# Performance work log

Measured on AMD Instinct MI355X. Metric: run time of the kernel, lower is better.

## Reference

```python
import jax, jax.numpy as jnp
import numpy as np

D_MODEL = 1024
NUM_HEADS = 16
D_K = D_MODEL // NUM_HEADS
TEMPERATURE = 1.0
EPS = 1e-6


def setup_inputs() -> dict:
    key = jax.random.key(0)
    ks = jax.random.split(key, 8)
    B, S, D, H = 2, 2048, D_MODEL, NUM_HEADS
    sc = 1.0 / np.sqrt(D)
    x = jax.random.normal(ks[0], (B, S, D), dtype=jnp.float32)
    Wq = jax.random.normal(ks[1], (D, D), dtype=jnp.float32) * sc
    Wk = jax.random.normal(ks[2], (D, D), dtype=jnp.float32) * sc
    Wv = jax.random.normal(ks[3], (D, D), dtype=jnp.float32) * sc
    Wo = jax.random.normal(ks[4], (D, D), dtype=jnp.float32) * sc
    bo = jnp.zeros((D,), dtype=jnp.float32)
    phase_scale = jnp.ones((H,), dtype=jnp.float32)
    # orthogonal init for entanglement matrix
    q, _ = np.linalg.qr(np.random.default_rng(0).normal(size=(H, H)))
    ent = jnp.asarray(q, dtype=jnp.float32)
    gamma = jnp.ones((D,), dtype=jnp.float32)
    beta = jnp.zeros((D,), dtype=jnp.float32)
    return {"x": x, "Wq": Wq, "Wk": Wk, "Wv": Wv, "Wo": Wo, "bo": bo,
            "phase_scale": phase_scale, "ent": ent, "gamma": gamma, "beta": beta}


def reference(x, Wq, Wk, Wv, Wo, bo, phase_scale, ent, gamma, beta):
    B, S, D = x.shape
    H, dk = NUM_HEADS, D_K
    # projections -> [B, H, S, dk]
    Q = (x @ Wq).reshape(B, S, H, dk).transpose(0, 2, 1, 3)
    K = (x @ Wk).reshape(B, S, H, dk).transpose(0, 2, 1, 3)
    V = (x @ Wv).reshape(B, S, H, dk).transpose(0, 2, 1, 3)
    # per-head QK^T, scaled, phase-modulated
    scores = jnp.einsum('bhqd,bhkd->bhqk', Q, K)
    inv = 1.0 / (float(np.sqrt(dk)) * TEMPERATURE)
    s = scores * (inv * phase_scale)[None, :, None, None]
    # real part of quantum phase: cos(s) + 0.1*cos(2s)  (imag part of V is zero,
    # so head_output = attended_real; the 0.1*attended_imag term vanishes)
    w = jnp.cos(s) + 0.1 * jnp.cos(2.0 * s)
    w = jax.nn.softmax(w, axis=-1)
    att = jnp.einsum('bhqk,bhkd->bhqd', w, V).transpose(0, 2, 1, 3)  # [B,S,H,dk]
    # faithful reproduction of tf.einsum('bsnd,hm->bsmd', ...): sums over n AND h
    att = jnp.einsum('bsnd,hm->bsmd', att, ent)
    out = att.reshape(B, S, D) @ Wo + bo
    r = out + x
    mu = jnp.mean(r, axis=-1, keepdims=True)
    var = jnp.mean(jnp.square(r - mu), axis=-1, keepdims=True)
    return gamma * (r - mu) * jax.lax.rsqrt(var + EPS) + beta
```

## Files before the change

kernel.cpp:

```cpp
#include <hip/hip_runtime.h>
#include <cstdint>
#include <cstddef>

#define S_LEN 2048
#define DMODEL 1024
#define NHEADS 16
#define DKH 64
#define MROWS 4096
#define BH_CNT 32

typedef __bf16 bf16x8 __attribute__((ext_vector_type(8)));
typedef __bf16 bf16x2 __attribute__((ext_vector_type(2)));
typedef float f32x4 __attribute__((ext_vector_type(4)));
typedef unsigned int u32x4 __attribute__((ext_vector_type(4)));
typedef unsigned int u32;
typedef unsigned short u16;

__device__ __forceinline__ u16 f2bfu(float f) {
  u32 u = __float_as_uint(f);
  return (u16)((u + 0x7FFFu + ((u >> 16) & 1u)) >> 16);
}

__device__ __forceinline__ u32 pk_bf16(float a, float b) {
  bf16x2 v;
  v[0] = (__bf16)a;
  v[1] = (__bf16)b;
  return __builtin_bit_cast(u32, v);
}

__device__ __forceinline__ void pl32swap(u32& a, u32& b) {
#if __has_builtin(__builtin_amdgcn_permlane32_swap)
  auto r = __builtin_amdgcn_permlane32_swap((int)a, (int)b, false, false);
  a = (u32)r[0]; b = (u32)r[1];
#else
  asm volatile("v_permlane32_swap_b32 %0, %1" : "+v"(a), "+v"(b));
#endif
}
__device__ __forceinline__ void pl16swap(u32& a, u32& b) {
#if __has_builtin(__builtin_amdgcn_permlane16_swap)
  auto r = __builtin_amdgcn_permlane16_swap((int)a, (int)b, false, false);
  a = (u32)r[0]; b = (u32)r[1];
#else
  asm volatile("v_permlane16_swap_b32 %0, %1" : "+v"(a), "+v"(b));
#endif
}

__device__ __forceinline__ void gload16(void* lds, const void* g) {
  __builtin_amdgcn_global_load_lds(
      (const __attribute__((address_space(1))) void*)g,
      (__attribute__((address_space(3))) void*)lds, 16, 0, 0);
}

__global__ __launch_bounds__(256) void prep_xb_k(const float* __restrict__ x,
                                                 u16* __restrict__ xb) {
  int i = (blockIdx.x * 256 + threadIdx.x) * 4;
  float4 v = *(const float4*)(x + i);
  *(uint2*)(xb + i) = make_uint2(pk_bf16(v.x, v.y), pk_bf16(v.z, v.w));
}

__global__ __launch_bounds__(256) void prep_w_k(const float* __restrict__ Wq,
    const float* __restrict__ Wk, const float* __restrict__ Wv,
    const float* __restrict__ ps, u16* __restrict__ Wb) {
  __shared__ float tile[32][33];
  int sel = blockIdx.z;
  const float* W = sel == 0 ? Wq : (sel == 1 ? Wk : Wv);
  int k0 = blockIdx.x * 32, c0 = blockIdx.y * 32;
  int tx = threadIdx.x, ty = threadIdx.y;
#pragma unroll
  for (int i = 0; i < 4; ++i)
    tile[ty + i * 8][tx] = W[(size_t)(k0 + ty + i * 8) * DMODEL + c0 + tx];
  __syncthreads();
#pragma unroll
  for (int i = 0; i < 4; ++i) {
    int row = ty + i * 8;
    float v = tile[tx][row];
    if (sel == 1) v *= 0.019894367886486918f * ps[(c0 + row) >> 6];
    Wb[(size_t)(sel * 1024 + c0 + row) * DMODEL + k0 + tx] = f2bfu(v);
  }
}

__global__ __launch_bounds__(256) void prep_woeff_k(const float* __restrict__ Wo,
    const float* __restrict__ ent, float* __restrict__ Woeff) {
  __shared__ float e[16];
  int t = threadIdx.x;
  if (t < 16) {
    float s = 0.f;
#pragma unroll
    for (int h = 0; h < 16; ++h) s += ent[h * 16 + t];
    e[t] = s;
  }
  __syncthreads();
  int gid = blockIdx.x * 256 + t;
  int d = gid >> 10, j = gid & 1023;
  float acc = 0.f;
#pragma unroll
  for (int m = 0; m < 16; ++m) acc += e[m] * Wo[(size_t)((m << 6) + d) * DMODEL + j];
  Woeff[(size_t)d * DMODEL + j] = acc;
}

__global__ __launch_bounds__(256) void gemm_qkv_k(const u16* __restrict__ xb,
    const u16* __restrict__ Wb, u16* __restrict__ Qb, u16* __restrict__ Kb,
    u16* __restrict__ Vt) {
  __shared__ __align__(16) u16 SMEM[2][2][128 * 32];
  int bid = blockIdx.x;
  int xcd = bid & 7, wi = bid >> 3;
  int mg = xcd >> 1, ng = xcd & 1;
  int mt = mg * 8 + (wi & 7);
  int nt = ng * 12 + (wi >> 3);
  int m0 = mt * 128, n0 = nt * 128;
  int tid = threadIdx.x;
  int lane = tid & 63, w = tid >> 6;
  int c = lane & 15, g = lane >> 4;
  int wr = w >> 1, wc = w & 1;

  int cij0 = (w * 2) * 64 + lane, cij1 = (w * 2 + 1) * 64 + lane;
  int row0 = cij0 >> 2, kp0 = (cij0 & 3) ^ (row0 & 3);
  int row1 = cij1 >> 2, kp1 = (cij1 & 3) ^ (row1 & 3);
  const u16* a0p = xb + (size_t)(m0 + row0) * DMODEL + kp0 * 8;
  const u16* a1p = xb + (size_t)(m0 + row1) * DMODEL + kp1 * 8;
  const u16* b0p = Wb + (size_t)(n0 + row0) * DMODEL + kp0 * 8;
  const u16* b1p = Wb + (size_t)(n0 + row1) * DMODEL + kp1 * 8;

  f32x4 acc[4][4];
#pragma unroll
  for (int i = 0; i < 4; ++i)
#pragma unroll
    for (int j = 0; j < 4; ++j) acc[i][j] = (f32x4){0.f, 0.f, 0.f, 0.f};

  gload16(&SMEM[0][0][(w * 2) * 512], a0p);
  gload16(&SMEM[0][0][(w * 2 + 1) * 512], a1p);
  gload16(&SMEM[1][0][(w * 2) * 512], b0p);
  gload16(&SMEM[1][0][(w * 2 + 1) * 512], b1p);
  __syncthreads();

  int cur = 0;
  for (int kt = 0; kt < DMODEL; kt += 32) {
    if (kt + 32 < DMODEL) {
      int nx = cur ^ 1, ko = kt + 32;
      gload16(&SMEM[0][nx][(w * 2) * 512], a0p + ko);
      gload16(&SMEM[0][nx][(w * 2 + 1) * 512], a1p + ko);
      gload16(&SMEM[1][nx][(w * 2) * 512], b0p + ko);
      gload16(&SMEM[1][nx][(w * 2 + 1) * 512], b1p + ko);
    }
    const u16* Ac = SMEM[0][cur];
    const u16* Bc = SMEM[1][cur];
    bf16x8 af[4], bf[4];
#pragma unroll
    for (int i = 0; i < 4; ++i) {
      int ra = wr * 64 + i * 16 + c;
      af[i] = *(const bf16x8*)(Ac + ra * 32 + ((g ^ (ra & 3)) * 8));
      int rb = wc * 64 + i * 16 + c;
      bf[i] = *(const bf16x8*)(Bc + rb * 32 + ((g ^ (rb & 3)) * 8));
    }
#pragma unroll
    for (int i = 0; i < 4; ++i)
#pragma unroll
      for (int j = 0; j < 4; ++j)
        acc[i][j] = __builtin_amdgcn_mfma_f32_16x16x32_bf16(af[i], bf[j], acc[i][j], 0, 0, 0);
    __syncthreads();
    cur ^= 1;
  }

  int sel = n0 >> 10;
  char* Ls = (char*)&SMEM[0][0][0];
  if (sel == 2) {
#pragma unroll
    for (int i = 0; i < 4; ++i)
#pragma unroll
      for (int jf = 0; jf < 4; ++jf) {
        int n = wc * 64 + jf * 16 + c;
        int m = wr * 64 + i * 16 + 4 * g;
        int byte = n * 256 + ((m * 2) ^ ((n & 7) << 4));
        *(uint2*)(Ls + byte) = make_uint2(pk_bf16(acc[i][jf][0], acc[i][jf][1]),
                                          pk_bf16(acc[i][jf][2], acc[i][jf][3]));
      }
  } else {
#pragma unroll
    for (int i = 0; i < 4; ++i)
#pragma unroll
      for (int jf = 0; jf < 4; ++jf) {
        int n = wc * 64 + jf * 16 + c;
#pragma unroll
        for (int j = 0; j < 4; ++j) {
          int m = wr * 64 + i * 16 + 4 * g + j;
          int byte = m * 256 + ((n * 2) ^ ((m & 7) << 4));
          __bf16 hv = (__bf16)acc[i][jf][j];
          *(u16*)(Ls + byte) = __builtin_bit_cast(u16, hv);
        }
      }
  }
  __syncthreads();
  int r = tid >> 1, half = tid & 1;
  int h0 = (n0 & 1023) >> 6;
  int b = m0 >> 11, sbase = m0 & 2047;
  u16* dst;
  if (sel == 2) {
    int bh = b * 16 + h0 + (r >> 6), d = r & 63;
    dst = Vt + ((size_t)bh * DKH + d) * S_LEN + sbase + half * 64;
  } else {
    u16* base = (sel == 0 ? Qb : Kb);
    int bh = b * 16 + h0 + half;
    dst = base + ((size_t)bh * S_LEN + sbase + r) * DKH;
  }
#pragma unroll
  for (int kk = 0; kk < 8; ++kk) {
    int byte = r * 256 + ((half * 128 + kk * 16) ^ ((r & 7) << 4));
    *(uint4*)(dst + kk * 8) = *(const uint4*)(Ls + byte);
  }
}

__global__ __launch_bounds__(512) void attn_k(const u16* __restrict__ Qb,
    const u16* __restrict__ Kb, const u16* __restrict__ Vt,
    float* __restrict__ attbuf) {
  __shared__ __align__(16) u16 Ks[2][4096];
  __shared__ __align__(16) u16 Vs[2][4096];
  __shared__ float dred[8][2][16];
  int fid = blockIdx.x;
  int swz = (fid & 7) * 64 + (fid >> 3);
  int bh = swz >> 4, qb = swz & 15;
  int tid = threadIdx.x;
  int lane = tid & 63, w = tid >> 6;
  int c = lane & 15, g = lane >> 4;
  int grp = w >> 2, h = (w >> 1) & 1, qh = w & 1;
  int q0 = qb * 128 + grp * 64;
  const float L2E = 1.4426950408889634f;

  const u16* Kbase = Kb + (size_t)bh * S_LEN * DKH;
  const u16* Vbase = Vt + (size_t)bh * DKH * S_LEN;

  int srow = w * 8 + (lane >> 3), slot = lane & 7, kp = slot ^ (srow & 7);
  const u16* kSrc = Kbase + (size_t)srow * DKH + kp * 8;
  const u16* vSrc = Vbase + (size_t)srow * S_LEN + kp * 8;
  auto stage = [&](int buf, int tile) {
    gload16(&Ks[buf][w * 512], kSrc + (size_t)tile * 64 * DKH);
    gload16(&Vs[buf][w * 512], vSrc + tile * 64);
  };

  int rot = qb * 2;
  stage(0, rot);

  bf16x8 qf[2][2];
#pragma unroll
  for (int qg = 0; qg < 2; ++qg) {
    const u16* qp = Qb + ((size_t)bh * S_LEN + q0 + qh * 32 + qg * 16 + c) * DKH + g * 8;
    qf[qg][0] = *(const bf16x8*)qp;
    qf[qg][1] = *(const bf16x8*)(qp + 32);
  }
  bf16x8 onesf;
#pragma unroll
  for (int i = 0; i < 8; ++i) onesf[i] = (__bf16)1.0f;

  const u16* kptr[2][2];
#pragma unroll
  for (int fm = 0; fm < 2; ++fm) {
    int row = h * 32 + fm * 16 + c;
    kptr[fm][0] = &Ks[0][row * 64 + ((g ^ (row & 7)) * 8)];
    kptr[fm][1] = &Ks[0][row * 64 + (((4 + g) ^ (row & 7)) * 8)];
  }
  const u16* vptr[4];
#pragma unroll
  for (int fd = 0; fd < 4; ++fd) {
    int vrow = fd * 16 + c;
    vptr[fd] = &Vs[0][vrow * 64 + (((4 * h + g) ^ (vrow & 7)) * 8)];
  }

  f32x4 attT[4][2];
#pragma unroll
  for (int i = 0; i < 4; ++i)
#pragma unroll
    for (int qg = 0; qg < 2; ++qg) attT[i][qg] = (f32x4){0.f, 0.f, 0.f, 0.f};
  f32x4 denacc[2];
  denacc[0] = (f32x4){0.f, 0.f, 0.f, 0.f};
  denacc[1] = (f32x4){0.f, 0.f, 0.f, 0.f};

  auto compute = [&](const int off) {
    f32x4 sT[2][2];
    __builtin_amdgcn_s_setprio(1);
#pragma unroll
    for (int fm = 0; fm < 2; ++fm) {
      bf16x8 a0 = *(const bf16x8*)(kptr[fm][0] + off);
      bf16x8 a1 = *(const bf16x8*)(kptr[fm][1] + off);
#pragma unroll
      for (int qg = 0; qg < 2; ++qg) {
        f32x4 z = (f32x4){0.f, 0.f, 0.f, 0.f};
        z = __builtin_amdgcn_mfma_f32_16x16x32_bf16(a0, qf[qg][0], z, 0, 0, 0);
        sT[fm][qg] = __builtin_amdgcn_mfma_f32_16x16x32_bf16(a1, qf[qg][1], z, 0, 0, 0);
      }
    }
    __builtin_amdgcn_s_setprio(0);
    u32 wq[2][2][2];
#pragma unroll
    for (int fm = 0; fm < 2; ++fm)
#pragma unroll
      for (int qg = 0; qg < 2; ++qg) {
        float pv[4];
#pragma unroll
        for (int j = 0; j < 4; ++j) {
          float cv = __builtin_amdgcn_cosf(sT[fm][qg][j]);
          float w2 = __fmaf_rn(cv, __fmaf_rn(0.2f * L2E, cv, L2E), -0.1f * L2E);
          pv[j] = __builtin_amdgcn_exp2f(w2);
        }
        wq[qg][fm][0] = pk_bf16(pv[0], pv[1]);
        wq[qg][fm][1] = pk_bf16(pv[2], pv[3]);
      }
    bf16x8 pf[2];
#pragma unroll
    for (int qg = 0; qg < 2; ++qg) {
      u32 b0 = wq[qg][0][0], b2 = wq[qg][1][0];
      pl32swap(b0, b2);
      pl16swap(b0, b2);
      u32 b1 = wq[qg][0][1], b3 = wq[qg][1][1];
      pl32swap(b1, b3);
      pl16swap(b1, b3);
      pf[qg] = __builtin_bit_cast(bf16x8, (u32x4){b0, b1, b2, b3});
    }
    __builtin_amdgcn_s_setprio(1);
#pragma unroll
    for (int fd = 0; fd < 4; ++fd) {
      bf16x8 vf = *(const bf16x8*)(vptr[fd] + off);
#pragma unroll
      for (int qg = 0; qg < 2; ++qg)
        attT[fd][qg] = __builtin_amdgcn_mfma_f32_16x16x32_bf16(vf, pf[qg], attT[fd][qg], 0, 0, 0);
    }
#pragma unroll
    for (int qg = 0; qg < 2; ++qg)
      denacc[qg] = __builtin_amdgcn_mfma_f32_16x16x32_bf16(onesf, pf[qg], denacc[qg], 0, 0, 0);
    __builtin_amdgcn_s_setprio(0);
  };

  __syncthreads();
  for (int t = 0; t < 32; t += 2) {
    stage(1, (t + 1 + rot) & 31);
    compute(0);
    __syncthreads();
    if (t + 2 < 32) stage(0, (t + 2 + rot) & 31);
    compute(4096);
    __syncthreads();
  }

  if (g == 0) {
    dred[w][0][c] = denacc[0][0];
    dred[w][1][c] = denacc[1][0];
  }
  float* Rq = (grp ? (float*)&Vs[0][0] : (float*)&Ks[0][0]) + qh * 2048;
  if (h == 1) {
#pragma unroll
    for (int fd = 0; fd < 4; ++fd)
#pragma unroll
      for (int qg = 0; qg < 2; ++qg)
        *(f32x4*)&Rq[(qg * 16 + c) * 64 + fd * 16 + 4 * g] = attT[fd][qg];
  }
  __syncthreads();
  if (h == 0) {
    float inv[2];
#pragma unroll
    for (int qg = 0; qg < 2; ++qg)
      inv[qg] = 1.f / (dred[w][qg][c] + dred[w ^ 2][qg][c]);
#pragma unroll
    for (int fd = 0; fd < 4; ++fd)
#pragma unroll
      for (int qg = 0; qg < 2; ++qg) {
        f32x4 part = *(const f32x4*)&Rq[(qg * 16 + c) * 64 + fd * 16 + 4 * g];
        f32x4 tot = (attT[fd][qg] + part) * inv[qg];
        int q = q0 + qh * 32 + qg * 16 + c;
        *(f32x4*)(attbuf + ((size_t)bh * S_LEN + q) * DKH + fd * 16 + 4 * g) = tot;
      }
  }
}

__global__ __launch_bounds__(256) void fuse_out_ln_k(const float* __restrict__ attbuf,
    const float* __restrict__ Woeff, const float* __restrict__ bo,
    const float* __restrict__ x, const float* __restrict__ gamma,
    const float* __restrict__ beta, float* __restrict__ out) {
  __shared__ float red[8][256];
  __shared__ __align__(16) float a[8][64];
  __shared__ float sred[8][4][2];
  int t = threadIdx.x;
  int r0 = blockIdx.x * 8;
  int d = t & 63, hg = t >> 6;
#pragma unroll
  for (int rr = 0; rr < 8; ++rr) {
    int m = r0 + rr, b = m >> 11, sr = m & 2047;
    float pa = 0.f;
#pragma unroll
    for (int hh = 0; hh < 4; ++hh) {
      int h = hg * 4 + hh;
      pa += attbuf[(((size_t)(b * 16 + h)) * S_LEN + sr) * DKH + d];
    }
    red[rr][t] = pa;
  }
  __syncthreads();
#pragma unroll
  for (int e = 0; e < 2; ++e) {
    int idx = t + e * 256;
    int rr = idx >> 6, dd = idx & 63;
    a[rr][dd] = red[rr][dd] + red[rr][64 + dd] + red[rr][128 + dd] + red[rr][192 + dd];
  }
  __syncthreads();

  float o[8][4];
#pragma unroll
  for (int rr = 0; rr < 8; ++rr) { o[rr][0] = o[rr][1] = o[rr][2] = o[rr][3] = 0.f; }
  int c4 = t * 4;
  for (int dd = 0; dd < 64; dd += 4) {
    float4 wv0 = *(const float4*)(Woeff + (size_t)(dd + 0) * DMODEL + c4);
    float4 wv1 = *(const float4*)(Woeff + (size_t)(dd + 1) * DMODEL + c4);
    float4 wv2 = *(const float4*)(Woeff + (size_t)(dd + 2) * DMODEL + c4);
    float4 wv3 = *(const float4*)(Woeff + (size_t)(dd + 3) * DMODEL + c4);
#pragma unroll
    for (int rr = 0; rr < 8; ++rr) {
      float4 av = *(const float4*)&a[rr][dd];
      o[rr][0] += av.x * wv0.x + av.y * wv1.x + av.z * wv2.x + av.w * wv3.x;
      o[rr][1] += av.x * wv0.y + av.y * wv1.y + av.z * wv2.y + av.w * wv3.y;
      o[rr][2] += av.x * wv0.z + av.y * wv1.z + av.z * wv2.z + av.w * wv3.z;
      o[rr][3] += av.x * wv0.w + av.y * wv1.w + av.z * wv2.w + av.w * wv3.w;
    }
  }
  float4 bv = *(const float4*)(bo + c4);
  int w = t >> 6, lane = t & 63;
#pragma unroll
  for (int rr = 0; rr < 8; ++rr) {
    int m = r0 + rr;
    float4 xv = *(const float4*)(x + (size_t)m * DMODEL + c4);
    o[rr][0] += bv.x + xv.x;
    o[rr][1] += bv.y + xv.y;
    o[rr][2] += bv.z + xv.z;
    o[rr][3] += bv.w + xv.w;
    float s = o[rr][0] + o[rr][1] + o[rr][2] + o[rr][3];
    float q = o[rr][0] * o[rr][0] + o[rr][1] * o[rr][1] + o[rr][2] * o[rr][2] + o[rr][3] * o[rr][3];
#pragma unroll
    for (int mm = 1; mm < 64; mm <<= 1) {
      s += __shfl_xor(s, mm, 64);
      q += __shfl_xor(q, mm, 64);
    }
    if (lane == 0) { sred[rr][w][0] = s; sred[rr][w][1] = q; }
  }
  __syncthreads();
  float4 gv = *(const float4*)(gamma + c4);
  float4 bev = *(const float4*)(beta + c4);
#pragma unroll
  for (int rr = 0; rr < 8; ++rr) {
    float s = sred[rr][0][0] + sred[rr][1][0] + sred[rr][2][0] + sred[rr][3][0];
    float q = sred[rr][0][1] + sred[rr][1][1] + sred[rr][2][1] + sred[rr][3][1];
    float mu = s * (1.f / 1024.f);
    float var = q * (1.f / 1024.f) - mu * mu;
    float rs = rsqrtf(var + 1e-6f);
    int m = r0 + rr;
    float4 ov;
    ov.x = gv.x * (o[rr][0] - mu) * rs + bev.x;
    ov.y = gv.y * (o[rr][1] - mu) * rs + bev.y;
    ov.z = gv.z * (o[rr][2] - mu) * rs + bev.z;
    ov.w = gv.w * (o[rr][3] - mu) * rs + bev.w;
    *(float4*)(out + (size_t)m * DMODEL + c4) = ov;
  }
}

extern "C" void kernel_launch(void* const* d_in, const int* in_sizes, int n_in,
                              void* d_out, int out_size, void* d_ws, size_t ws_size,
                              hipStream_t stream) {
  const float* x = (const float*)d_in[0];
  const float* Wq = (const float*)d_in[1];
  const float* Wk = (const float*)d_in[2];
  const float* Wv = (const float*)d_in[3];
  const float* Wo = (const float*)d_in[4];
  const float* bo = (const float*)d_in[5];
  const float* ps = (const float*)d_in[6];
  const float* ent = (const float*)d_in[7];
  const float* gamma = (const float*)d_in[8];
  const float* beta = (const float*)d_in[9];
  float* out = (float*)d_out;

  char* ws = (char*)d_ws;
  size_t o = 0;
  u16* xb = (u16*)(ws + o);    o += (size_t)MROWS * DMODEL * 2;
  u16* Wb = (u16*)(ws + o);    o += (size_t)3072 * 1024 * 2;
  u16* Qb = (u16*)(ws + o);    o += (size_t)BH_CNT * S_LEN * DKH * 2;
  u16* Kb = (u16*)(ws + o);    o += (size_t)BH_CNT * S_LEN * DKH * 2;
  u16* Vt = (u16*)(ws + o);    o += (size_t)BH_CNT * S_LEN * DKH * 2;
  float* Woeff = (float*)(ws + o);  o += (size_t)DKH * DMODEL * 4;
  float* attbuf = (float*)(ws + o); o += (size_t)BH_CNT * S_LEN * DKH * 4;

  prep_xb_k<<<dim3(4096), dim3(256), 0, stream>>>(x, xb);
  prep_w_k<<<dim3(32, 32, 3), dim3(32, 8), 0, stream>>>(Wq, Wk, Wv, ps, Wb);
  prep_woeff_k<<<dim3(256), dim3(256), 0, stream>>>(Wo, ent, Woeff);
  gemm_qkv_k<<<dim3(768), dim3(256), 0, stream>>>(xb, Wb, Qb, Kb, Vt);
  attn_k<<<dim3(512), dim3(512), 0, stream>>>(Qb, Kb, Vt, attbuf);
  fuse_out_ln_k<<<dim3(512), dim3(256), 0, stream>>>(attbuf, Woeff, bo, x, gamma, beta, out);
}
```

Baseline: 129.0 us.

## Merge prep kernels, deepen attention K/V staging, store attention output as bf16

The three preprocessing kernels become one launch that dispatches on block index, which removes two kernel launch gaps. The attention kernel moves from double to four-buffer K/V staging, loading two tiles ahead and syncing once per two tiles, which doubles LDS use and may lower occupancy. The intermediate attention output is written and read as bf16 instead of fp32, halving that buffer's traffic at some cost in precision.

```diff
diff --git a/kernel.cpp b/kernel.cpp
--- a/kernel.cpp
+++ b/kernel.cpp
@@ -19,6 +19,10 @@
 __device__ __forceinline__ u16 f2bfu(float f) {
   u32 u = __float_as_uint(f);
   return (u16)((u + 0x7FFFu + ((u >> 16) & 1u)) >> 16);
+}
+
+__device__ __forceinline__ float bf2f(u16 v) {
+  return __uint_as_float((u32)v << 16);
 }
 
 __device__ __forceinline__ u32 pk_bf16(float a, float b) {
@@ -51,51 +55,51 @@
       (__attribute__((address_space(3))) void*)lds, 16, 0, 0);
 }
 
-__global__ __launch_bounds__(256) void prep_xb_k(const float* __restrict__ x,
-                                                 u16* __restrict__ xb) {
-  int i = (blockIdx.x * 256 + threadIdx.x) * 4;
-  float4 v = *(const float4*)(x + i);
-  *(uint2*)(xb + i) = make_uint2(pk_bf16(v.x, v.y), pk_bf16(v.z, v.w));
-}
-
-__global__ __launch_bounds__(256) void prep_w_k(const float* __restrict__ Wq,
-    const float* __restrict__ Wk, const float* __restrict__ Wv,
-    const float* __restrict__ ps, u16* __restrict__ Wb) {
+__global__ __launch_bounds__(256) void prep_all_k(const float* __restrict__ x,
+    const float* __restrict__ Wq, const float* __restrict__ Wk,
+    const float* __restrict__ Wv, const float* __restrict__ Wo,
+    const float* __restrict__ ps, const float* __restrict__ ent,
+    u16* __restrict__ xb, u16* __restrict__ Wb, float* __restrict__ Woeff) {
   __shared__ float tile[32][33];
-  int sel = blockIdx.z;
-  const float* W = sel == 0 ? Wq : (sel == 1 ? Wk : Wv);
-  int k0 = blockIdx.x * 32, c0 = blockIdx.y * 32;
-  int tx = threadIdx.x, ty = threadIdx.y;
-#pragma unroll
-  for (int i = 0; i < 4; ++i)
-    tile[ty + i * 8][tx] = W[(size_t)(k0 + ty + i * 8) * DMODEL + c0 + tx];
-  __syncthreads();
-#pragma unroll
-  for (int i = 0; i < 4; ++i) {
-    int row = ty + i * 8;
-    float v = tile[tx][row];
-    if (sel == 1) v *= 0.019894367886486918f * ps[(c0 + row) >> 6];
-    Wb[(size_t)(sel * 1024 + c0 + row) * DMODEL + k0 + tx] = f2bfu(v);
-  }
-}
-
-__global__ __launch_bounds__(256) void prep_woeff_k(const float* __restrict__ Wo,
-    const float* __restrict__ ent, float* __restrict__ Woeff) {
-  __shared__ float e[16];
+  int bid = blockIdx.x;
   int t = threadIdx.x;
-  if (t < 16) {
-    float s = 0.f;
-#pragma unroll
-    for (int h = 0; h < 16; ++h) s += ent[h * 16 + t];
-    e[t] = s;
-  }
-  __syncthreads();
-  int gid = blockIdx.x * 256 + t;
-  int d = gid >> 10, j = gid & 1023;
-  float acc = 0.f;
-#pragma unroll
-  for (int m = 0; m < 16; ++m) acc += e[m] * Wo[(size_t)((m << 6) + d) * DMODEL + j];
-  Woeff[(size_t)d * DMODEL + j] = acc;
+  if (bid < 4096) {
+    int i = (bid * 256 + t) * 4;
+    float4 v = *(const float4*)(x + i);
+    *(uint2*)(xb + i) = make_uint2(pk_bf16(v.x, v.y), pk_bf16(v.z, v.w));
+  } else if (bid < 7168) {
+    int lb = bid - 4096;
+    int sel = lb >> 10, rem = lb & 1023;
+    int k0 = (rem & 31) * 32, c0 = (rem >> 5) * 32;
+    const float* W = sel == 0 ? Wq : (sel == 1 ? Wk : Wv);
+    int tx = t & 31, ty = t >> 5;
+#pragma unroll
+    for (int i = 0; i < 4; ++i)
+      tile[ty + i * 8][tx] = W[(size_t)(k0 + ty + i * 8) * DMODEL + c0 + tx];
+    __syncthreads();
+#pragma unroll
+    for (int i = 0; i < 4; ++i) {
+      int row = ty + i * 8;
+      float v = tile[tx][row];
+      if (sel == 1) v *= 0.019894367886486918f * ps[(c0 + row) >> 6];
+      Wb[(size_t)(sel * 1024 + c0 + row) * DMODEL + k0 + tx] = f2bfu(v);
+    }
+  } else {
+    __shared__ float e[16];
+    if (t < 16) {
+      float s = 0.f;
+#pragma unroll
+      for (int h = 0; h < 16; ++h) s += ent[h * 16 + t];
+      e[t] = s;
+    }
+    __syncthreads();
+    int gid = (bid - 7168) * 256 + t;
+    int d = gid >> 10, j = gid & 1023;
+    float acc = 0.f;
+#pragma unroll
+    for (int m = 0; m < 16; ++m) acc += e[m] * Wo[(size_t)((m << 6) + d) * DMODEL + j];
+    Woeff[(size_t)d * DMODEL + j] = acc;
+  }
 }
 
 __global__ __launch_bounds__(256) void gemm_qkv_k(const u16* __restrict__ xb,
@@ -211,9 +215,9 @@
 
 __global__ __launch_bounds__(512) void attn_k(const u16* __restrict__ Qb,
     const u16* __restrict__ Kb, const u16* __restrict__ Vt,
-    float* __restrict__ attbuf) {
-  __shared__ __align__(16) u16 Ks[2][4096];
-  __shared__ __align__(16) u16 Vs[2][4096];
+    u16* __restrict__ attbufb) {
+  __shared__ __align__(16) u16 Ks[4][4096];
+  __shared__ __align__(16) u16 Vs[4][4096];
   __shared__ float dred[8][2][16];
   int fid = blockIdx.x;
   int swz = (fid & 7) * 64 + (fid >> 3);
@@ -237,7 +241,8 @@
   };
 
   int rot = qb * 2;
-  stage(0, rot);
+  stage(0, rot & 31);
+  stage(1, (rot + 1) & 31);
 
   bf16x8 qf[2][2];
 #pragma unroll
@@ -329,12 +334,18 @@
   };
 
   __syncthreads();
-  for (int t = 0; t < 32; t += 2) {
-    stage(1, (t + 1 + rot) & 31);
+  for (int t = 0; t < 32; t += 4) {
+    stage(2, (t + 2 + rot) & 31);
+    stage(3, (t + 3 + rot) & 31);
     compute(0);
+    compute(4096);
     __syncthreads();
-    if (t + 2 < 32) stage(0, (t + 2 + rot) & 31);
-    compute(4096);
+    if (t + 4 < 32) {
+      stage(0, (t + 4 + rot) & 31);
+      stage(1, (t + 5 + rot) & 31);
+    }
+    compute(8192);
+    compute(12288);
     __syncthreads();
   }
 
@@ -363,12 +374,13 @@
         f32x4 part = *(const f32x4*)&Rq[(qg * 16 + c) * 64 + fd * 16 + 4 * g];
         f32x4 tot = (attT[fd][qg] + part) * inv[qg];
         int q = q0 + qh * 32 + qg * 16 + c;
-        *(f32x4*)(attbuf + ((size_t)bh * S_LEN + q) * DKH + fd * 16 + 4 * g) = tot;
+        *(uint2*)(attbufb + ((size_t)bh * S_LEN + q) * DKH + fd * 16 + 4 * g) =
+            make_uint2(pk_bf16(tot[0], tot[1]), pk_bf16(tot[2], tot[3]));
       }
   }
 }
 
-__global__ __launch_bounds__(256) void fuse_out_ln_k(const float* __restrict__ attbuf,
+__global__ __launch_bounds__(256) void fuse_out_ln_k(const u16* __restrict__ attbufb,
     const float* __restrict__ Woeff, const float* __restrict__ bo,
     const float* __restrict__ x, const float* __restrict__ gamma,
     const float* __restrict__ beta, float* __restrict__ out) {
@@ -385,7 +397,7 @@
 #pragma unroll
     for (int hh = 0; hh < 4; ++hh) {
       int h = hg * 4 + hh;
-      pa += attbuf[(((size_t)(b * 16 + h)) * S_LEN + sr) * DKH + d];
+      pa += bf2f(attbufb[(((size_t)(b * 16 + h)) * S_LEN + sr) * DKH + d]);
     }
     red[rr][t] = pa;
   }
@@ -477,13 +489,12 @@
   u16* Qb = (u16*)(ws + o);    o += (size_t)BH_CNT * S_LEN * DKH * 2;
   u16* Kb = (u16*)(ws + o);    o += (size_t)BH_CNT * S_LEN * DKH * 2;
   u16* Vt = (u16*)(ws + o);    o += (size_t)BH_CNT * S_LEN * DKH * 2;
-  float* Woeff = (float*)(ws + o);  o += (size_t)DKH * DMODEL * 4;
-  float* attbuf = (float*)(ws + o); o += (size_t)BH_CNT * S_LEN * DKH * 4;
-
-  prep_xb_k<<<dim3(4096), dim3(256), 0, stream>>>(x, xb);
-  prep_w_k<<<dim3(32, 32, 3), dim3(32, 8), 0, stream>>>(Wq, Wk, Wv, ps, Wb);
-  prep_woeff_k<<<dim3(256), dim3(256), 0, stream>>>(Wo, ent, Woeff);
+  float* Woeff = (float*)(ws + o);   o += (size_t)DKH * DMODEL * 4;
+  u16* attbufb = (u16*)(ws + o);     o += (size_t)BH_CNT * S_LEN * DKH * 2;
+
+  prep_all_k<<<dim3(7424), dim3(256), 0, stream>>>(x, Wq, Wk, Wv, Wo, ps, ent,
+                                                   xb, Wb, Woeff);
   gemm_qkv_k<<<dim3(768), dim3(256), 0, stream>>>(xb, Wb, Qb, Kb, Vt);
-  attn_k<<<dim3(512), dim3(512), 0, stream>>>(Qb, Kb, Vt, attbuf);
-  fuse_out_ln_k<<<dim3(512), dim3(256), 0, stream>>>(attbuf, Woeff, bo, x, gamma, beta, out);
-}
+  attn_k<<<dim3(512), dim3(512), 0, stream>>>(Qb, Kb, Vt, attbufb);
+  fuse_out_ln_k<<<dim3(512), dim3(256), 0, stream>>>(attbufb, Woeff, bo, x, gamma, beta, out);
+}
```

After: 123.7 us. 4.1% less time.
